# Kernel tuning notes

Hardware: AMD Instinct MI355X
Metric: run time of the kernel (lower is better)

The kernel has to match this reference:

```python
import jax, jax.numpy as jnp
import numpy as np

N = 100000          # nodes
E = 3_200_000       # edges (avg degree 32)
F_IN = 1433
H1, C1 = 8, 8       # conv1: 8 heads x 8 channels -> 64 concat
H2, C2 = 1, 7       # conv2: 1 head x 7 classes
NEG_SLOPE = 0.2


def setup_inputs() -> dict:
    key = jax.random.key(0)
    ks = jax.random.split(key, 10)
    x = jax.random.normal(ks[0], (N, F_IN), dtype=jnp.float32)
    edge_index = jax.random.randint(ks[1], (2, E), 0, N, dtype=jnp.int64)
    s1 = 1.0 / np.sqrt(F_IN)
    s2 = 1.0 / np.sqrt(H1 * C1)
    return {
        "x": x,
        "edge_index": edge_index,
        "W1": jax.random.normal(ks[2], (F_IN, H1 * C1), dtype=jnp.float32) * s1,
        "att_src1": jax.random.normal(ks[3], (H1, C1), dtype=jnp.float32) * s2,
        "att_dst1": jax.random.normal(ks[4], (H1, C1), dtype=jnp.float32) * s2,
        "b1": jnp.zeros((H1 * C1,), dtype=jnp.float32),
        "W2": jax.random.normal(ks[5], (H1 * C1, H2 * C2), dtype=jnp.float32) * s2,
        "att_src2": jax.random.normal(ks[6], (H2, C2), dtype=jnp.float32),
        "att_dst2": jax.random.normal(ks[7], (H2, C2), dtype=jnp.float32),
        "b2": jnp.zeros((H2 * C2,), dtype=jnp.float32),
    }


def gat_conv(x, src, dst, W, att_src, att_dst, b, heads, ch):
    # x: [N, F_in]; src/dst: [E'] (self-loops already appended)
    h = (x @ W).reshape(N, heads, ch)                     # [N, H, C]
    a_src = jnp.einsum('nhc,hc->nh', h, att_src)          # [N, H]
    a_dst = jnp.einsum('nhc,hc->nh', h, att_dst)
    e = a_src[src] + a_dst[dst]                           # [E', H]
    e = jax.nn.leaky_relu(e, NEG_SLOPE)
    # segment softmax over incoming edges of each dst node
    m = jax.ops.segment_max(e, dst, num_segments=N)       # [N, H]
    w = jnp.exp(e - m[dst])
    denom = jax.ops.segment_sum(w, dst, num_segments=N)   # [N, H]
    alpha = w / denom[dst]                                # [E', H]
    msg = alpha[:, :, None] * h[src]                      # [E', H, C]
    out = jax.ops.segment_sum(msg, dst, num_segments=N)   # [N, H, C]
    return out.reshape(N, heads * ch) + b


def reference(x, edge_index, W1, att_src1, att_dst1, b1, W2, att_src2, att_dst2, b2):
    loops = jnp.arange(N, dtype=edge_index.dtype)
    src = jnp.concatenate([edge_index[0], loops])
    dst = jnp.concatenate([edge_index[1], loops])
    # eval mode: all dropout layers are identity
    h = gat_conv(x, src, dst, W1, att_src1, att_dst1, b1, H1, C1)   # [N, 64]
    h = jax.nn.elu(h)
    h = gat_conv(h, src, dst, W2, att_src2, att_dst2, b2, H2, C2)   # [N, 7]
    return jax.nn.log_softmax(h, axis=1)
```

## Files before the change

kernel.cpp:

```cpp
#include <hip/hip_runtime.h>
#include <hip/hip_bf16.h>
#include <math.h>

#define NN 100000
#define EE 3200000
#define ET (EE + NN)
#define FIN 1433
#define KPAD 1440
#define NT 45
#define F1 64
#define F2 7
#define NB 391
#define G1B 782
#define SB 1024
#define CAP 128

typedef __attribute__((ext_vector_type(8))) short short8;
typedef __attribute__((ext_vector_type(4))) float f32x4;

static __device__ __forceinline__ unsigned short f2bf(float f) {
  __hip_bfloat16 h = __float2bfloat16(f);
  return *reinterpret_cast<unsigned short*>(&h);
}
static __device__ __forceinline__ float bf2f(unsigned short u) {
  return __uint_as_float((unsigned int)u << 16);
}

__global__ __launch_bounds__(256) void k_prep(const float* __restrict__ W1,
                                              int* __restrict__ cnt,
                                              unsigned short* __restrict__ WT) {
  int i = blockIdx.x * 256 + threadIdx.x;
  if (i < NN) cnt[i] = 0;
  if (i < F1 * KPAD) {
    int c = i / KPAD, k = i - c * KPAD;
    WT[i] = f2bf((k < FIN) ? W1[k * F1 + c] : 0.f);
  }
}

#define BM 128
#define AROWB 80
#define ABYTES (BM * AROWB)
#define BBYTES 4096
#define BUFB (ABYTES + BBYTES)

__global__ __launch_bounds__(256) void k_fuse1(const float* __restrict__ X,
                                               const unsigned short* __restrict__ WT,
                                               unsigned short* __restrict__ Hb,
                                               const int* __restrict__ ei,
                                               int* __restrict__ cnt,
                                               int* __restrict__ csr) {
  if (blockIdx.x >= G1B) {
    const int stride = SB * 256;
    for (int e = (blockIdx.x - G1B) * 256 + threadIdx.x; e < ET; e += stride) {
      int src, dst;
      if (e < EE) { src = ei[e]; dst = ei[EE + e]; }
      else        { src = e - EE; dst = src; }
      int pos = atomicAdd(&cnt[dst], 1);
      csr[(dst << 7) + pos] = src;
    }
    return;
  }
  __shared__ __align__(16) char smem[2 * BUFB];
  const int tid = threadIdx.x;
  const int lane = tid & 63;
  const int w = tid >> 6;
  const int row0 = blockIdx.x * BM;
  const int wr = (w >> 1) * 64;
  const int wc = (w & 1) * 32;
  const int l15 = lane & 15, l4 = lane >> 4;

  int arow[2], akc[2];
  const float* asrc[2];
#pragma unroll
  for (int q = 0; q < 2; ++q) {
    int chunk = q * 256 + tid;
    arow[q] = chunk >> 2;
    akc[q] = chunk & 3;
    int gr = row0 + arow[q];
    if (gr >= NN) gr = NN - 1;
    asrc[q] = X + (size_t)gr * FIN + akc[q] * 8;
  }
  const unsigned short* bsrc =
      WT + (tid >> 2) * KPAD + (((tid & 3) ^ ((tid >> 3) & 3)) << 3);

  f32x4 acc[4][2];
#pragma unroll
  for (int a = 0; a < 4; ++a)
#pragma unroll
    for (int b = 0; b < 2; ++b) acc[a][b] = 0.f;

  float av[2][8];
  short8 bv;

  auto loadAB = [&](int k0) {
    bool kfull = (k0 + 32 <= FIN);
#pragma unroll
    for (int q = 0; q < 2; ++q) {
      if (kfull) {
#pragma unroll
        for (int e = 0; e < 8; ++e) av[q][e] = asrc[q][k0 + e];
      } else {
#pragma unroll
        for (int e = 0; e < 8; ++e) {
          int gk = k0 + akc[q] * 8 + e;
          av[q][e] = (gk < FIN) ? asrc[q][k0 + e] : 0.f;
        }
      }
    }
    bv = *(const short8*)(bsrc + k0);
  };

  auto stage = [&](char* buf) {
#pragma unroll
    for (int q = 0; q < 2; ++q) {
      short8 v;
#pragma unroll
      for (int e = 0; e < 8; ++e) v[e] = (short)f2bf(av[q][e]);
      *(short8*)(buf + arow[q] * AROWB + akc[q] * 16) = v;
    }
    *(short8*)(buf + ABYTES + tid * 16) = bv;
  };

  loadAB(0);
  stage(smem);
  __syncthreads();

  int cur = 0;
  for (int t = 0; t < NT; ++t) {
    if (t + 1 < NT) loadAB((t + 1) * 32);
    char* buf = smem + cur * BUFB;
    short8 af[4], bf[2];
#pragma unroll
    for (int fr = 0; fr < 4; ++fr)
      af[fr] = *(const short8*)(buf + (wr + fr * 16 + l15) * AROWB + l4 * 16);
#pragma unroll
    for (int fc = 0; fc < 2; ++fc) {
      int c = wc + fc * 16 + l15;
      int jp = l4 ^ ((c >> 1) & 3);
      bf[fc] = *(const short8*)(buf + ABYTES + c * 64 + jp * 16);
    }
#pragma unroll
    for (int fr = 0; fr < 4; ++fr)
#pragma unroll
      for (int fc = 0; fc < 2; ++fc)
        acc[fr][fc] = __builtin_amdgcn_mfma_f32_16x16x32_bf16(
            af[fr], bf[fc], acc[fr][fc], 0, 0, 0);
    if (t + 1 < NT) stage(smem + (cur ^ 1) * BUFB);
    __syncthreads();
    cur ^= 1;
  }

#pragma unroll
  for (int fr = 0; fr < 4; ++fr) {
    int rbase = row0 + wr + fr * 16 + l4 * 4;
#pragma unroll
    for (int q = 0; q < 4; ++q) {
      int r = rbase + q;
      if (r < NN) {
#pragma unroll
        for (int fc = 0; fc < 2; ++fc)
          Hb[(size_t)r * F1 + wc + fc * 16 + l15] = f2bf(acc[fr][fc][q]);
      }
    }
  }
}

__global__ __launch_bounds__(256) void k_att1(const unsigned short* __restrict__ Hb,
                                              const float* __restrict__ attS,
                                              const float* __restrict__ attD,
                                              float* __restrict__ aS,
                                              float* __restrict__ aD) {
  __shared__ float s_s[64], s_d[64];
  if (threadIdx.x < 64) { s_s[threadIdx.x] = attS[threadIdx.x]; s_d[threadIdx.x] = attD[threadIdx.x]; }
  __syncthreads();
  int idx = blockIdx.x * 256 + threadIdx.x;
  int n = idx >> 3, h = idx & 7;
  if (n >= NN) return;
  short8 v8 = *(const short8*)(Hb + (size_t)n * 64 + h * 8);
  float ss = 0.f, dd = 0.f;
#pragma unroll
  for (int c = 0; c < 8; ++c) {
    float v = bf2f((unsigned short)v8[c]);
    ss = fmaf(v, s_s[h * 8 + c], ss);
    dd = fmaf(v, s_d[h * 8 + c], dd);
  }
  aS[n * 8 + h] = ss;
  aD[n * 8 + h] = dd;
}

__global__ __launch_bounds__(256) void k_agg1(const unsigned short* __restrict__ Hb,
                                              const float* __restrict__ aS,
                                              const float* __restrict__ aD,
                                              const int* __restrict__ cnt,
                                              const int* __restrict__ csr,
                                              const float* __restrict__ b1,
                                              const float* __restrict__ W2,
                                              const float* __restrict__ s2,
                                              const float* __restrict__ d2,
                                              unsigned short* __restrict__ H2b,
                                              float* __restrict__ aD2) {
  __shared__ float s_w2[448];
  __shared__ float s_ss[7], s_dd[7];
  __shared__ float s_b1[64];
  for (int i = threadIdx.x; i < 448; i += 256) s_w2[i] = W2[i];
  if (threadIdx.x < 7) { s_ss[threadIdx.x] = s2[threadIdx.x]; s_dd[threadIdx.x] = d2[threadIdx.x]; }
  if (threadIdx.x < 64) s_b1[threadIdx.x] = b1[threadIdx.x];
  __syncthreads();

  const int wv = threadIdx.x >> 6, lane = threadIdx.x & 63;
  const int n = blockIdx.x * 4 + wv;
  if (n >= NN) return;
  const int eg = lane >> 3, q = lane & 7;
  const float adv = aD[n * 8 + q];
  const int beg = n << 7;
  const int deg = cnt[n];
  float acc[8] = {};
  float den = 0.f;
#pragma unroll 2
  for (int i = eg; i < deg; i += 8) {
    int s = csr[beg + i];
    float e = aS[s * 8 + q] + adv;
    e = (e > 0.f) ? e : 0.2f * e;
    float w = __expf(e);
    den += w;
    short8 hv = *(const short8*)(Hb + (size_t)s * 64 + q * 8);
#pragma unroll
    for (int c = 0; c < 8; ++c)
      acc[c] = fmaf(w, bf2f((unsigned short)hv[c]), acc[c]);
  }
#pragma unroll
  for (int off = 8; off < 64; off <<= 1) {
    den += __shfl_xor(den, off, 64);
#pragma unroll
    for (int c = 0; c < 8; ++c) acc[c] += __shfl_xor(acc[c], off, 64);
  }
  if (eg == 0) {
    float inv = 1.f / den;
    float v[8];
#pragma unroll
    for (int c = 0; c < 8; ++c) {
      float t = acc[c] * inv + s_b1[q * 8 + c];
      v[c] = (t > 0.f) ? t : (__expf(t) - 1.f);
    }
    float p[7] = {};
#pragma unroll
    for (int c = 0; c < 8; ++c) {
      const float* wr = &s_w2[(q * 8 + c) * 7];
#pragma unroll
      for (int j = 0; j < 7; ++j) p[j] = fmaf(v[c], wr[j], p[j]);
    }
#pragma unroll
    for (int off = 1; off < 8; off <<= 1) {
#pragma unroll
      for (int j = 0; j < 7; ++j) p[j] += __shfl_xor(p[j], off, 64);
    }
    if (q == 0) {
      float s = 0.f, d = 0.f;
      short8 row;
#pragma unroll
      for (int j = 0; j < 7; ++j) {
        row[j] = (short)f2bf(p[j]);
        s = fmaf(p[j], s_ss[j], s);
        d = fmaf(p[j], s_dd[j], d);
      }
      row[7] = (short)f2bf(s);
      *(short8*)(H2b + (size_t)n * 8) = row;
      aD2[n] = d;
    }
  }
}

__global__ __launch_bounds__(256) void k_agg2(const unsigned short* __restrict__ H2b,
                                              const float* __restrict__ aD2,
                                              const int* __restrict__ cnt,
                                              const int* __restrict__ csr,
                                              const float* __restrict__ b2,
                                              float* __restrict__ out) {
  const int wv = threadIdx.x >> 6, lane = threadIdx.x & 63;
  const int n = blockIdx.x * 4 + wv;
  if (n >= NN) return;
  const float adv = aD2[n];
  const int beg = n << 7;
  const int deg = cnt[n];
  float acc[7] = {};
  float den = 0.f;
  for (int j = lane; j < deg; j += 64) {
    int s = csr[beg + j];
    short8 hv = *(const short8*)(H2b + (size_t)s * 8);
    float e = bf2f((unsigned short)hv[7]) + adv;
    e = (e > 0.f) ? e : 0.2f * e;
    float wgt = __expf(e);
    den += wgt;
#pragma unroll
    for (int c = 0; c < 7; ++c)
      acc[c] = fmaf(wgt, bf2f((unsigned short)hv[c]), acc[c]);
  }
#pragma unroll
  for (int off = 32; off > 0; off >>= 1) {
    den += __shfl_xor(den, off, 64);
#pragma unroll
    for (int c = 0; c < 7; ++c) acc[c] += __shfl_xor(acc[c], off, 64);
  }
  if (lane == 0) {
    float inv = 1.f / den;
    float v[7];
    float m = -1e30f;
#pragma unroll
    for (int c = 0; c < 7; ++c) { v[c] = acc[c] * inv + b2[c]; m = fmaxf(m, v[c]); }
    float se = 0.f;
#pragma unroll
    for (int c = 0; c < 7; ++c) se += __expf(v[c] - m);
    float lse = m + __logf(se);
#pragma unroll
    for (int c = 0; c < 7; ++c) out[n * 7 + c] = v[c] - lse;
  }
}

extern "C" void kernel_launch(void* const* d_in, const int* in_sizes, int n_in,
                              void* d_out, int out_size, void* d_ws, size_t ws_size,
                              hipStream_t stream) {
  const float* x   = (const float*)d_in[0];
  const int*   ei  = (const int*)d_in[1];
  const float* W1  = (const float*)d_in[2];
  const float* as1 = (const float*)d_in[3];
  const float* ad1 = (const float*)d_in[4];
  const float* b1  = (const float*)d_in[5];
  const float* W2  = (const float*)d_in[6];
  const float* as2 = (const float*)d_in[7];
  const float* ad2 = (const float*)d_in[8];
  const float* b2  = (const float*)d_in[9];
  float* out = (float*)d_out;

  char* ws = (char*)d_ws;
  size_t off = 0;
  auto alloc = [&](size_t bytes) {
    void* p = ws + off;
    off += (bytes + 255) & ~(size_t)255;
    return p;
  };
  unsigned short* h1b = (unsigned short*)alloc((size_t)NN * 64 * 2);
  float* sc1    = (float*)alloc((size_t)NN * 8 * 4);
  float* dc1    = (float*)alloc((size_t)NN * 8 * 4);
  unsigned short* h2b = (unsigned short*)alloc((size_t)NN * 8 * 2);
  float* dc2    = (float*)alloc((size_t)NN * 4);
  int*   cnt    = (int*)alloc((size_t)NN * 4);
  int*   csr    = (int*)alloc((size_t)NN * CAP * 4);
  unsigned short* w1t = (unsigned short*)alloc((size_t)F1 * KPAD * 2);

  k_prep<<<NB, 256, 0, stream>>>(W1, cnt, w1t);

  k_fuse1<<<G1B + SB, 256, 0, stream>>>(x, w1t, h1b, ei, cnt, csr);

  k_att1<<<(NN * 8 + 255) / 256, 256, 0, stream>>>(h1b, as1, ad1, sc1, dc1);

  k_agg1<<<(NN + 3) / 4, 256, 0, stream>>>(h1b, sc1, dc1, cnt, csr, b1,
                                           W2, as2, ad2, h2b, dc2);

  k_agg2<<<(NN + 3) / 4, 256, 0, stream>>>(h2b, dc2, cnt, csr, b2, out);
}
```

Before: 449.0 us.

## Stage fp32 X tiles directly into LDS via global_load_lds, convert on read

The first-layer GEMM used to load fp32 X through registers, convert to bf16 and write it to LDS. It now issues asynchronous direct-to-LDS 16-byte loads of the raw fp32 tile into an XOR-swizzled layout, and converts to bf16 when building the MFMA fragments. The ragged last K tile is still loaded through registers with masking. This frees registers and VGPR traffic and lets loads overlap with MFMA, at the cost of doubling the LDS tile size and relying on correct waitcnt handling for the async LDS writes.

```diff
diff --git a/kernel.cpp b/kernel.cpp
--- a/kernel.cpp
+++ b/kernel.cpp
@@ -17,6 +17,8 @@
 
 typedef __attribute__((ext_vector_type(8))) short short8;
 typedef __attribute__((ext_vector_type(4))) float f32x4;
+typedef __attribute__((address_space(3))) unsigned int u32_lds;
+typedef __attribute__((address_space(1))) const unsigned int u32_glb;
 
 static __device__ __forceinline__ unsigned short f2bf(float f) {
   __hip_bfloat16 h = __float2bfloat16(f);
@@ -38,10 +40,9 @@
 }
 
 #define BM 128
-#define AROWB 80
-#define ABYTES (BM * AROWB)
-#define BBYTES 4096
-#define BUFB (ABYTES + BBYTES)
+#define TILEA 16384
+#define TILEB 4096
+#define BUFB (TILEA + TILEB)
 
 __global__ __launch_bounds__(256) void k_fuse1(const float* __restrict__ X,
                                                const unsigned short* __restrict__ WT,
@@ -63,22 +64,22 @@
   __shared__ __align__(16) char smem[2 * BUFB];
   const int tid = threadIdx.x;
   const int lane = tid & 63;
-  const int w = tid >> 6;
+  const int wid = tid >> 6;
   const int row0 = blockIdx.x * BM;
-  const int wr = (w >> 1) * 64;
-  const int wc = (w & 1) * 32;
+  const int wr = (wid >> 1) * 64;
+  const int wc = (wid & 1) * 32;
   const int l15 = lane & 15, l4 = lane >> 4;
 
-  int arow[2], akc[2];
-  const float* asrc[2];
-#pragma unroll
-  for (int q = 0; q < 2; ++q) {
-    int chunk = q * 256 + tid;
-    arow[q] = chunk >> 2;
-    akc[q] = chunk & 3;
-    int gr = row0 + arow[q];
-    if (gr >= NN) gr = NN - 1;
-    asrc[q] = X + (size_t)gr * FIN + akc[q] * 8;
+  const int lrq = tid >> 3;
+  const int mq = tid & 7;
+  const char* Xb = (const char*)X;
+  size_t aoff[4];
+#pragma unroll
+  for (int q = 0; q < 4; ++q) {
+    int lr = q * 32 + lrq;
+    int gr = row0 + lr; if (gr >= NN) gr = NN - 1;
+    int c = mq ^ (lr & 7);
+    aoff[q] = (size_t)gr * (FIN * 4) + (size_t)c * 16;
   }
   const unsigned short* bsrc =
       WT + (tid >> 2) * KPAD + (((tid & 3) ^ ((tid >> 3) & 3)) << 3);
@@ -89,55 +90,69 @@
 #pragma unroll
     for (int b = 0; b < 2; ++b) acc[a][b] = 0.f;
 
-  float av[2][8];
-  short8 bv;
-
-  auto loadAB = [&](int k0) {
-    bool kfull = (k0 + 32 <= FIN);
-#pragma unroll
-    for (int q = 0; q < 2; ++q) {
-      if (kfull) {
-#pragma unroll
-        for (int e = 0; e < 8; ++e) av[q][e] = asrc[q][k0 + e];
-      } else {
-#pragma unroll
-        for (int e = 0; e < 8; ++e) {
-          int gk = k0 + akc[q] * 8 + e;
-          av[q][e] = (gk < FIN) ? asrc[q][k0 + e] : 0.f;
-        }
-      }
-    }
-    bv = *(const short8*)(bsrc + k0);
+  auto gstage = [&](int k0, char* buf) {
+#pragma unroll
+    for (int q = 0; q < 4; ++q) {
+      __builtin_amdgcn_global_load_lds(
+          (u32_glb*)(Xb + aoff[q] + (size_t)k0 * 4),
+          (u32_lds*)(buf + q * 4096 + wid * 1024), 16, 0, 0);
+    }
   };
 
-  auto stage = [&](char* buf) {
-#pragma unroll
-    for (int q = 0; q < 2; ++q) {
-      short8 v;
-#pragma unroll
-      for (int e = 0; e < 8; ++e) v[e] = (short)f2bf(av[q][e]);
-      *(short8*)(buf + arow[q] * AROWB + akc[q] * 16) = v;
-    }
-    *(short8*)(buf + ABYTES + tid * 16) = bv;
-  };
-
-  loadAB(0);
-  stage(smem);
+  gstage(0, smem);
+  {
+    short8 b0 = *(const short8*)(bsrc + 0);
+    *(short8*)(smem + TILEA + tid * 16) = b0;
+  }
   __syncthreads();
 
   int cur = 0;
   for (int t = 0; t < NT; ++t) {
-    if (t + 1 < NT) loadAB((t + 1) * 32);
     char* buf = smem + cur * BUFB;
+    char* nbuf = smem + (cur ^ 1) * BUFB;
+    const bool have_next = (t + 1 < NT);
+    const bool tail = (t + 1 == NT - 1);
+    short8 bnext;
+    f32x4 atail[4];
+    if (have_next) {
+      if (!tail) {
+        gstage((t + 1) * 32, nbuf);
+      } else {
+#pragma unroll
+        for (int q = 0; q < 4; ++q) {
+          int lr = q * 32 + lrq;
+          int gr = row0 + lr; if (gr >= NN) gr = NN - 1;
+          int c = mq ^ (lr & 7);
+          int kb = (NT - 1) * 32 + c * 4;
+          const float* xp = X + (size_t)gr * FIN + kb;
+#pragma unroll
+          for (int j = 0; j < 4; ++j)
+            atail[q][j] = (kb + j < FIN) ? xp[j] : 0.f;
+        }
+      }
+      bnext = *(const short8*)(bsrc + (t + 1) * 32);
+    }
+
     short8 af[4], bf[2];
-#pragma unroll
-    for (int fr = 0; fr < 4; ++fr)
-      af[fr] = *(const short8*)(buf + (wr + fr * 16 + l15) * AROWB + l4 * 16);
+    const int sz = l15 & 7;
+#pragma unroll
+    for (int fr = 0; fr < 4; ++fr) {
+      int r = wr + fr * 16 + l15;
+      f32x4 a0 = *(const f32x4*)(buf + r * 128 + ((2 * l4) ^ sz) * 16);
+      f32x4 a1 = *(const f32x4*)(buf + r * 128 + ((2 * l4 + 1) ^ sz) * 16);
+      short8 v;
+#pragma unroll
+      for (int j = 0; j < 4; ++j) {
+        v[j] = (short)f2bf(a0[j]);
+        v[4 + j] = (short)f2bf(a1[j]);
+      }
+      af[fr] = v;
+    }
 #pragma unroll
     for (int fc = 0; fc < 2; ++fc) {
       int c = wc + fc * 16 + l15;
       int jp = l4 ^ ((c >> 1) & 3);
-      bf[fc] = *(const short8*)(buf + ABYTES + c * 64 + jp * 16);
+      bf[fc] = *(const short8*)(buf + TILEA + c * 64 + jp * 16);
     }
 #pragma unroll
     for (int fr = 0; fr < 4; ++fr)
@@ -145,7 +160,15 @@
       for (int fc = 0; fc < 2; ++fc)
         acc[fr][fc] = __builtin_amdgcn_mfma_f32_16x16x32_bf16(
             af[fr], bf[fc], acc[fr][fc], 0, 0, 0);
-    if (t + 1 < NT) stage(smem + (cur ^ 1) * BUFB);
+
+    if (have_next) {
+      if (tail) {
+#pragma unroll
+        for (int q = 0; q < 4; ++q)
+          *(f32x4*)(nbuf + (q * 32 + lrq) * 128 + mq * 16) = atail[q];
+      }
+      *(short8*)(nbuf + TILEA + tid * 16) = bnext;
+    }
     __syncthreads();
     cur ^= 1;
   }
```

After: 438.6 us. 2.3% less time.
